# Performance work log

Measured on AMD Instinct MI355X. Metric: run time of the kernel, lower is better.

## Reference

```python
import jax, jax.numpy as jnp
import numpy as np
import math

D_MODEL = 2048
N_HEADS = 16
D_HEAD = D_MODEL // N_HEADS
D_FF = 8192
B = 2
S = 2048
LN_EPS = 1e-5


def _rope_tables(s, d_head):
    inv_freq = 1.0 / (10000.0 ** (np.arange(0, d_head, 2, dtype=np.float32) / d_head))
    t = np.arange(s, dtype=np.float32)
    freqs = np.outer(t, inv_freq)                      # [s, d_head/2]
    emb = np.concatenate([freqs, freqs], axis=-1)      # [s, d_head]
    cos = jnp.asarray(np.cos(emb))[None, None]         # [1,1,s,d_head]
    sin = jnp.asarray(np.sin(emb))[None, None]
    return cos, sin


def setup_inputs() -> dict:
    key = jax.random.key(0)
    ks = jax.random.split(key, 12)
    x = jax.random.normal(ks[0], (B, S, D_MODEL), dtype=jnp.float32)
    cos, sin = _rope_tables(S, D_HEAD)
    # additive causal mask
    mask = jnp.where(jnp.tril(jnp.ones((S, S), dtype=bool)), 0.0, -1e9).astype(jnp.float32)[None, None]
    s_in = 1.0 / math.sqrt(D_MODEL)
    s_ff = 1.0 / math.sqrt(D_FF)
    params = {
        "ln1_g": jnp.ones((D_MODEL,), jnp.float32),
        "ln1_b": jnp.zeros((D_MODEL,), jnp.float32),
        "w_qkv": jax.random.uniform(ks[1], (D_MODEL, 3 * D_MODEL), jnp.float32, -s_in, s_in),
        "b_qkv": jax.random.uniform(ks[2], (3 * D_MODEL,), jnp.float32, -s_in, s_in),
        "w_out": jax.random.uniform(ks[3], (D_MODEL, D_MODEL), jnp.float32, -s_in, s_in),
        "b_out": jax.random.uniform(ks[4], (D_MODEL,), jnp.float32, -s_in, s_in),
        "ln2_g": jnp.ones((D_MODEL,), jnp.float32),
        "ln2_b": jnp.zeros((D_MODEL,), jnp.float32),
        "w_ff1": jax.random.uniform(ks[5], (D_MODEL, D_FF), jnp.float32, -s_in, s_in),
        "b_ff1": jax.random.uniform(ks[6], (D_FF,), jnp.float32, -s_in, s_in),
        "w_ff2": jax.random.uniform(ks[7], (D_FF, D_MODEL), jnp.float32, -s_ff, s_ff),
        "b_ff2": jax.random.uniform(ks[8], (D_MODEL,), jnp.float32, -s_ff, s_ff),
    }
    return {"x": x, "cos": cos, "sin": sin, "mask": mask, **params}


def _layernorm(x, g, b):
    m = jnp.mean(x, axis=-1, keepdims=True)
    v = jnp.var(x, axis=-1, keepdims=True)
    return (x - m) * jax.lax.rsqrt(v + LN_EPS) * g + b


def _rotate_half(x):
    x1, x2 = jnp.split(x, 2, axis=-1)
    return jnp.concatenate([-x2, x1], axis=-1)


def reference(x, cos, sin, mask,
              ln1_g, ln1_b, w_qkv, b_qkv, w_out, b_out,
              ln2_g, ln2_b, w_ff1, b_ff1, w_ff2, b_ff2):
    b, s, d = x.shape
    # attention sub-block (dropout = identity, eval mode)
    xn = _layernorm(x, ln1_g, ln1_b)
    qkv = (xn @ w_qkv + b_qkv).reshape(b, s, 3, N_HEADS, D_HEAD)
    qkv = jnp.transpose(qkv, (2, 0, 3, 1, 4))           # [3,b,h,s,dh]
    q, k, v = qkv[0], qkv[1], qkv[2]
    q = q * cos + _rotate_half(q) * sin
    k = k * cos + _rotate_half(k) * sin
    scale = 1.0 / math.sqrt(D_HEAD)
    attn = jnp.einsum('bhqd,bhkd->bhqk', q, k) * scale + mask
    attn = jax.nn.softmax(attn, axis=-1)
    a_out = jnp.einsum('bhqk,bhkd->bhqd', attn, v)
    a_out = jnp.transpose(a_out, (0, 2, 1, 3)).reshape(b, s, d)
    x = x + (a_out @ w_out + b_out)
    # MLP sub-block (exact GELU, matching torch nn.GELU default)
    xn = _layernorm(x, ln2_g, ln2_b)
    h = jax.nn.gelu(xn @ w_ff1 + b_ff1, approximate=False)
    x = x + (h @ w_ff2 + b_ff2)
    return x
```

## Files before the change

### kernel.cpp

```cpp
#include <hip/hip_runtime.h>
#include <hip/hip_bf16.h>
#include <math.h>

typedef __hip_bfloat16 bf16;
using bf16x8 = __bf16 __attribute__((ext_vector_type(8)));
using f32x4  = float  __attribute__((ext_vector_type(4)));

#define D_MODEL 2048
#define S_LEN   2048
#define NB      2
#define NH      16
#define DHEAD   128
#define DFF     8192
#define M_ROWS  (NB * S_LEN)

__device__ __forceinline__ void gload_lds16(const void* g, void* l) {
    __builtin_amdgcn_global_load_lds((const __attribute__((address_space(1))) void*)g,
                                     (__attribute__((address_space(3))) void*)l, 16, 0, 0);
}

__global__ __launch_bounds__(256) void ln_kernel(const float* __restrict__ x,
                                                 const float* __restrict__ gw,
                                                 const float* __restrict__ bw,
                                                 bf16* __restrict__ out) {
    const int row = blockIdx.x;
    const float* xr = x + (size_t)row * D_MODEL;
    const int tid = threadIdx.x;
    float4 v0 = ((const float4*)xr)[tid * 2];
    float4 v1 = ((const float4*)xr)[tid * 2 + 1];
    float s = v0.x + v0.y + v0.z + v0.w + v1.x + v1.y + v1.z + v1.w;
    float q = v0.x*v0.x + v0.y*v0.y + v0.z*v0.z + v0.w*v0.w
            + v1.x*v1.x + v1.y*v1.y + v1.z*v1.z + v1.w*v1.w;
    #pragma unroll
    for (int off = 32; off; off >>= 1) {
        s += __shfl_xor(s, off);
        q += __shfl_xor(q, off);
    }
    __shared__ float red[8];
    const int wid = tid >> 6;
    if ((tid & 63) == 0) { red[wid] = s; red[4 + wid] = q; }
    __syncthreads();
    s = red[0] + red[1] + red[2] + red[3];
    q = red[4] + red[5] + red[6] + red[7];
    const float mean = s * (1.0f / D_MODEL);
    const float var  = q * (1.0f / D_MODEL) - mean * mean;
    const float inv  = rsqrtf(var + 1e-5f);
    float4 g0 = ((const float4*)gw)[tid * 2];
    float4 g1 = ((const float4*)gw)[tid * 2 + 1];
    float4 b0 = ((const float4*)bw)[tid * 2];
    float4 b1 = ((const float4*)bw)[tid * 2 + 1];
    bf16* orow = out + (size_t)row * D_MODEL + tid * 8;
    orow[0] = __float2bfloat16((v0.x - mean) * inv * g0.x + b0.x);
    orow[1] = __float2bfloat16((v0.y - mean) * inv * g0.y + b0.y);
    orow[2] = __float2bfloat16((v0.z - mean) * inv * g0.z + b0.z);
    orow[3] = __float2bfloat16((v0.w - mean) * inv * g0.w + b0.w);
    orow[4] = __float2bfloat16((v1.x - mean) * inv * g1.x + b1.x);
    orow[5] = __float2bfloat16((v1.y - mean) * inv * g1.y + b1.y);
    orow[6] = __float2bfloat16((v1.z - mean) * inv * g1.z + b1.z);
    orow[7] = __float2bfloat16((v1.w - mean) * inv * g1.w + b1.w);
}

__global__ __launch_bounds__(256) void transpose_f2b(const float* __restrict__ in,
                                                     bf16* __restrict__ out,
                                                     int R, int C) {
    __shared__ float t[32][33];
    const int c0 = blockIdx.x * 32, r0 = blockIdx.y * 32;
    const int tx = threadIdx.x & 31, ty = threadIdx.x >> 5;
    #pragma unroll
    for (int i = ty; i < 32; i += 8) t[i][tx] = in[(size_t)(r0 + i) * C + c0 + tx];
    __syncthreads();
    #pragma unroll
    for (int i = ty; i < 32; i += 8)
        out[(size_t)(c0 + i) * R + r0 + tx] = __float2bfloat16(t[tx][i]);
}

__global__ __launch_bounds__(256) void transpose_v(const bf16* __restrict__ in,
                                                   bf16* __restrict__ out) {
    const int bh = blockIdx.z;
    const bf16* ib = in + (size_t)bh * S_LEN * DHEAD;
    bf16* ob = out + (size_t)bh * DHEAD * S_LEN;
    __shared__ float t[32][33];
    const int c0 = blockIdx.x * 32;
    const int r0 = blockIdx.y * 32;
    const int tx = threadIdx.x & 31, ty = threadIdx.x >> 5;
    #pragma unroll
    for (int i = ty; i < 32; i += 8)
        t[i][tx] = __bfloat162float(ib[(size_t)(r0 + i) * DHEAD + c0 + tx]);
    __syncthreads();
    #pragma unroll
    for (int i = ty; i < 32; i += 8)
        ob[(size_t)(c0 + i) * S_LEN + r0 + tx] = __float2bfloat16(t[tx][i]);
}

__global__ __launch_bounds__(256) void rope_kernel(bf16* __restrict__ qk,
                                                   const float* __restrict__ ct,
                                                   const float* __restrict__ st) {
    const size_t idx = (size_t)blockIdx.x * 256 + threadIdx.x;
    const int dh = (int)(idx & 63);
    const size_t rrow = idx >> 6;
    const int sidx = (int)(rrow & (S_LEN - 1));
    const int which = (int)(rrow >> 16);
    const float f = (which == 0) ? 0.08838834764831845f : 1.0f;
    bf16* p = qk + rrow * DHEAD;
    const float c  = ct[sidx * DHEAD + dh];
    const float sn = st[sidx * DHEAD + dh];
    const float x1 = __bfloat162float(p[dh]);
    const float x2 = __bfloat162float(p[dh + 64]);
    p[dh]      = __float2bfloat16((x1 * c - x2 * sn) * f);
    p[dh + 64] = __float2bfloat16((x2 * c + x1 * sn) * f);
}

template <int EPI>
__global__ __launch_bounds__(256) void gemm_kernel(const bf16* __restrict__ A,
                                                   const bf16* __restrict__ Bt,
                                                   const float* __restrict__ bias,
                                                   const float* __restrict__ resid,
                                                   void* __restrict__ outp,
                                                   int M, int N, int K, int kLen) {
    __shared__ __align__(16) bf16 As[128][64];
    __shared__ __align__(16) bf16 Bs[128][64];
    const int tid  = threadIdx.x;
    const int lane = tid & 63;
    const int wid  = tid >> 6;
    const int wr = wid >> 1, wc = wid & 1;
    const int cc = lane & 15, g = lane >> 4;
    const int csw = cc & 7;

    const int nx = gridDim.x, ny = gridDim.y, nz = gridDim.z;
    int flat = blockIdx.x + nx * (blockIdx.y + ny * blockIdx.z);
    const int nwg = nx * ny * nz;
    flat = (flat & 7) * (nwg >> 3) + (flat >> 3);
    const int bx = flat % nx;
    const int t2 = flat / nx;
    const int by = t2 % ny;
    const int bz = t2 / ny;
    const int m0 = by * 128, n0 = bx * 128;
    const int kStart = bz * kLen;

    const int srow  = lane >> 3;
    const int sslot = (lane & 7) ^ (srow & 7);
    const int sb    = sslot * 16;

    f32x4 acc[4][4];
    const f32x4 zero = {0.f, 0.f, 0.f, 0.f};
    #pragma unroll
    for (int i = 0; i < 4; i++)
        #pragma unroll
        for (int j = 0; j < 4; j++) acc[i][j] = zero;

    const char* gA = (const char*)A  + ((size_t)(m0 + wid * 32 + srow) * K) * 2 + sb;
    const char* gB = (const char*)Bt + ((size_t)(n0 + wid * 32 + srow) * K) * 2 + sb;
    char* lA = (char*)&As[0][0] + wid * 4096;
    char* lB = (char*)&Bs[0][0] + wid * 4096;
    const size_t rowK2 = (size_t)K * 2;

    for (int k0 = kStart; k0 < kStart + kLen; k0 += 64) {
        #pragma unroll
        for (int c = 0; c < 4; ++c) {
            gload_lds16(gA + (size_t)k0 * 2 + (size_t)c * 8 * rowK2, lA + c * 1024);
            gload_lds16(gB + (size_t)k0 * 2 + (size_t)c * 8 * rowK2, lB + c * 1024);
        }
        __syncthreads();
        #pragma unroll
        for (int kh = 0; kh < 2; kh++) {
            const int ux = ((kh * 4 + g) ^ csw) << 4;
            bf16x8 af[4], bfm[4];
            #pragma unroll
            for (int mi = 0; mi < 4; mi++)
                af[mi]  = *(const bf16x8*)((const char*)&As[wr * 64 + mi * 16 + cc][0] + ux);
            #pragma unroll
            for (int ni = 0; ni < 4; ni++)
                bfm[ni] = *(const bf16x8*)((const char*)&Bs[wc * 64 + ni * 16 + cc][0] + ux);
            #pragma unroll
            for (int mi = 0; mi < 4; mi++)
                #pragma unroll
                for (int ni = 0; ni < 4; ni++)
                    acc[mi][ni] = __builtin_amdgcn_mfma_f32_16x16x32_bf16(af[mi], bfm[ni], acc[mi][ni], 0, 0, 0);
        }
        __syncthreads();
    }

    #pragma unroll
    for (int mi = 0; mi < 4; mi++) {
        #pragma unroll
        for (int ni = 0; ni < 4; ni++) {
            const int colb = n0 + wc * 64 + ni * 16 + cc;
            const float bcol = (EPI == 3) ? 0.0f : bias[colb];
            #pragma unroll
            for (int r = 0; r < 4; r++) {
                const int row = m0 + wr * 64 + mi * 16 + g * 4 + r;
                const float v = acc[mi][ni][r] + bcol;
                if (EPI == 0) {
                    const int which = colb >> 11;
                    const int h     = (colb >> 7) & 15;
                    const int dh    = colb & 127;
                    const int b     = row >> 11;
                    const int sidx  = row & (S_LEN - 1);
                    bf16* o = (bf16*)outp;
                    o[((size_t)(which * 32 + b * 16 + h) * S_LEN + sidx) * DHEAD + dh] = __float2bfloat16(v);
                } else if (EPI == 1) {
                    float* o = (float*)outp;
                    o[(size_t)row * N + colb] = v + resid[(size_t)row * N + colb];
                } else if (EPI == 2) {
                    bf16* o = (bf16*)outp;
                    const float gel = 0.5f * v * (1.0f + erff(v * 0.70710678118f));
                    o[(size_t)row * N + colb] = __float2bfloat16(gel);
                } else {
                    float* o = (float*)outp + (size_t)bz * M * N;
                    o[(size_t)row * N + colb] = v;
                }
            }
        }
    }
}

__global__ __launch_bounds__(256) void ff2_combine(const float* __restrict__ p,
                                                   const float* __restrict__ bias,
                                                   float* __restrict__ out) {
    const size_t i4 = (size_t)blockIdx.x * 256 + threadIdx.x;
    const float4 a  = ((const float4*)out)[i4];
    const float4 p0 = ((const float4*)p)[i4];
    const float4 p1 = ((const float4*)(p + (size_t)M_ROWS * D_MODEL))[i4];
    const float4 b  = ((const float4*)bias)[i4 & (D_MODEL / 4 - 1)];
    float4 r;
    r.x = a.x + p0.x + p1.x + b.x;
    r.y = a.y + p0.y + p1.y + b.y;
    r.z = a.z + p0.z + p1.z + b.z;
    r.w = a.w + p0.w + p1.w + b.w;
    ((float4*)out)[i4] = r;
}

__global__ __launch_bounds__(256) void attn_kernel(const bf16* __restrict__ q,
                                                   const bf16* __restrict__ k,
                                                   const bf16* __restrict__ vT,
                                                   bf16* __restrict__ aout) {
    int flat = blockIdx.x + gridDim.x * blockIdx.y;
    const int nwg = gridDim.x * gridDim.y;
    flat = (flat & 7) * (nwg >> 3) + (flat >> 3);
    const int qt = (int)(gridDim.x - 1 - (flat % gridDim.x));
    const int bh = flat / gridDim.x;
    const int tid = threadIdx.x;
    const int lane = tid & 63, wid = tid >> 6;
    const int cc = lane & 15, g = lane >> 4;
    const int csw = cc & 7;
    const int q0 = qt * 64;
    const int q0w = q0 + wid * 16;
    const bf16* qb = q  + (size_t)bh * S_LEN * DHEAD;
    const char* kb2 = (const char*)(k  + (size_t)bh * S_LEN * DHEAD);
    const char* vb2 = (const char*)(vT + (size_t)bh * DHEAD * S_LEN);

    __shared__ __align__(16) bf16 Ks[2][64][128];
    __shared__ __align__(16) bf16 Vs[2][128][64];
    __shared__ __align__(16) bf16 Ps[4][16][72];

    const int kst_row = wid * 4 + (lane >> 4);
    const int kst_sl  = (lane & 15) ^ (kst_row & 7);
    const int vst_row = wid * 8 + (lane >> 3);
    const int vst_sl  = (lane & 7) ^ (vst_row & 7);

    bf16x8 qf[4];
    #pragma unroll
    for (int kk = 0; kk < 4; kk++)
        qf[kk] = *(const bf16x8*)(qb + (size_t)(q0w + cc) * DHEAD + kk * 32 + g * 8);

    f32x4 oacc[8];
    const f32x4 zero = {0.f, 0.f, 0.f, 0.f};
    #pragma unroll
    for (int d = 0; d < 8; d++) oacc[d] = zero;
    float lsum[4] = {0.f, 0.f, 0.f, 0.f};

    {
        char* ksl = (char*)&Ks[0][0][0] + wid * 1024;
        char* vsl = (char*)&Vs[0][0][0] + wid * 1024;
        #pragma unroll
        for (int i = 0; i < 4; ++i) {
            gload_lds16(kb2 + (size_t)(kst_row + i * 16) * 256 + kst_sl * 16, ksl + i * 4096);
            gload_lds16(vb2 + (size_t)(vst_row + i * 32) * (S_LEN * 2) + vst_sl * 16, vsl + i * 4096);
        }
    }
    asm volatile("s_waitcnt vmcnt(0)" ::: "memory");
    __syncthreads();

    int cur = 0;
    for (int kt = 0; kt <= qt; ++kt) {
        const int kv0 = kt * 64;
        if (kt < qt) {
            const int nv0 = kv0 + 64;
            char* ksl = (char*)&Ks[cur ^ 1][0][0] + wid * 1024;
            char* vsl = (char*)&Vs[cur ^ 1][0][0] + wid * 1024;
            #pragma unroll
            for (int i = 0; i < 4; ++i) {
                gload_lds16(kb2 + (size_t)(nv0 + kst_row + i * 16) * 256 + kst_sl * 16, ksl + i * 4096);
                gload_lds16(vb2 + (size_t)(vst_row + i * 32) * (S_LEN * 2) + (size_t)nv0 * 2 + vst_sl * 16, vsl + i * 4096);
            }
        }

        f32x4 sacc[4];
        #pragma unroll
        for (int ni = 0; ni < 4; ni++) sacc[ni] = zero;
        __builtin_amdgcn_s_setprio(1);
        #pragma unroll
        for (int kk = 0; kk < 4; kk++) {
            const int ux = ((kk * 4 + g) ^ csw) << 4;
            #pragma unroll
            for (int ni = 0; ni < 4; ni++) {
                const bf16x8 kf = *(const bf16x8*)((const char*)&Ks[cur][ni * 16 + cc][0] + ux);
                sacc[ni] = __builtin_amdgcn_mfma_f32_16x16x32_bf16(qf[kk], kf, sacc[ni], 0, 0, 0);
            }
        }
        __builtin_amdgcn_s_setprio(0);

        #pragma unroll
        for (int r = 0; r < 4; r++) {
            const int qrow = q0w + g * 4 + r;
            float p[4];
            #pragma unroll
            for (int ni = 0; ni < 4; ni++) {
                const float sv = (kv0 + ni * 16 + cc <= qrow) ? sacc[ni][r] : -1e30f;
                p[ni] = __expf(sv);
            }
            lsum[r] += (p[0] + p[1]) + (p[2] + p[3]);
            #pragma unroll
            for (int ni = 0; ni < 4; ni++)
                Ps[wid][g * 4 + r][ni * 16 + cc] = __float2bfloat16(p[ni]);
        }

        __builtin_amdgcn_s_setprio(1);
        #pragma unroll
        for (int ks = 0; ks < 2; ks++) {
            const bf16x8 pf = *(const bf16x8*)(&Ps[wid][cc][ks * 32 + g * 8]);
            const int ux = ((ks * 4 + g) ^ csw) << 4;
            #pragma unroll
            for (int d = 0; d < 8; d++) {
                const bf16x8 vf = *(const bf16x8*)((const char*)&Vs[cur][d * 16 + cc][0] + ux);
                oacc[d] = __builtin_amdgcn_mfma_f32_16x16x32_bf16(pf, vf, oacc[d], 0, 0, 0);
            }
        }
        __builtin_amdgcn_s_setprio(0);

        asm volatile("s_waitcnt vmcnt(0)" ::: "memory");
        __syncthreads();
        cur ^= 1;
    }

    const int b = bh >> 4, h = bh & 15;
    #pragma unroll
    for (int r = 0; r < 4; r++) {
        float rs = lsum[r];
        #pragma unroll
        for (int off = 1; off < 16; off <<= 1) rs += __shfl_xor(rs, off);
        const float invl = 1.0f / rs;
        const int srow = q0w + g * 4 + r;
        bf16* orow = aout + ((size_t)(b * S_LEN + srow)) * D_MODEL + h * DHEAD;
        #pragma unroll
        for (int d = 0; d < 8; d++) orow[d * 16 + cc] = __float2bfloat16(oacc[d][r] * invl);
    }
}

extern "C" void kernel_launch(void* const* d_in, const int* in_sizes, int n_in,
                              void* d_out, int out_size, void* d_ws, size_t ws_size,
                              hipStream_t stream) {
    (void)in_sizes; (void)n_in; (void)out_size; (void)ws_size;
    const float* x      = (const float*)d_in[0];
    const float* cosb   = (const float*)d_in[1];
    const float* sinb   = (const float*)d_in[2];
    const float* ln1_g  = (const float*)d_in[4];
    const float* ln1_b  = (const float*)d_in[5];
    const float* w_qkv  = (const float*)d_in[6];
    const float* b_qkv  = (const float*)d_in[7];
    const float* w_out  = (const float*)d_in[8];
    const float* b_out  = (const float*)d_in[9];
    const float* ln2_g  = (const float*)d_in[10];
    const float* ln2_b  = (const float*)d_in[11];
    const float* w_ff1  = (const float*)d_in[12];
    const float* b_ff1  = (const float*)d_in[13];
    const float* w_ff2  = (const float*)d_in[14];
    const float* b_ff2  = (const float*)d_in[15];
    float* out = (float*)d_out;

    char* ws = (char*)d_ws;
    bf16* wT_qkv = (bf16*)(ws + 0);
    bf16* wT_out = (bf16*)(ws + 25165824);
    bf16* wT_ff1 = (bf16*)(ws + 33554432);
    bf16* wT_ff2 = (bf16*)(ws + 67108864);
    bf16* xn     = (bf16*)(ws + 100663296);
    bf16* qkv    = (bf16*)(ws + 117440512);
    bf16* aoutb  = (bf16*)(ws + 167772160);
    bf16* vTb    = (bf16*)(ws + 184549376);
    bf16* hbuf   = (bf16*)(ws + 117440512);
    float* partial = (float*)(ws + 0);
    bf16* kbuf = qkv + (size_t)32 * S_LEN * DHEAD;
    bf16* vbuf = qkv + (size_t)64 * S_LEN * DHEAD;

    transpose_f2b<<<dim3(192, 64),  256, 0, stream>>>(w_qkv, wT_qkv, 2048, 6144);
    transpose_f2b<<<dim3(64, 64),   256, 0, stream>>>(w_out, wT_out, 2048, 2048);
    transpose_f2b<<<dim3(256, 64),  256, 0, stream>>>(w_ff1, wT_ff1, 2048, 8192);
    transpose_f2b<<<dim3(64, 256),  256, 0, stream>>>(w_ff2, wT_ff2, 8192, 2048);

    ln_kernel<<<M_ROWS, 256, 0, stream>>>(x, ln1_g, ln1_b, xn);
    gemm_kernel<0><<<dim3(48, 32), 256, 0, stream>>>(xn, wT_qkv, b_qkv, nullptr, qkv, M_ROWS, 6144, 2048, 2048);
    rope_kernel<<<32768, 256, 0, stream>>>(qkv, cosb, sinb);
    transpose_v<<<dim3(4, 64, 32), 256, 0, stream>>>(vbuf, vTb);
    attn_kernel<<<dim3(32, 32), 256, 0, stream>>>(qkv, kbuf, vTb, aoutb);
    gemm_kernel<1><<<dim3(16, 32), 256, 0, stream>>>(aoutb, wT_out, b_out, x, out, M_ROWS, 2048, 2048, 2048);
    ln_kernel<<<M_ROWS, 256, 0, stream>>>(out, ln2_g, ln2_b, xn);
    gemm_kernel<2><<<dim3(64, 32), 256, 0, stream>>>(xn, wT_ff1, b_ff1, nullptr, hbuf, M_ROWS, DFF, 2048, 2048);
    gemm_kernel<3><<<dim3(16, 32, 2), 256, 0, stream>>>(hbuf, wT_ff2, nullptr, nullptr, partial, M_ROWS, 2048, 8192, 4096);
    ff2_combine<<<8192, 256, 0, stream>>>(partial, b_ff2, out);
}
```

Before: 799.4 us.

## Add 256x256-tile GEMM kernel with 8 waves and phased LDS pipelining

Adds a new gemm256 kernel that uses 256x256 output tiles with 512 threads, double-buffered LDS filled by direct global-to-LDS loads, XOR swizzling, and a workgroup index remap for cache locality. Each K-step is split into four phases that overlap MFMA compute with staging the next tile, using explicit vmcnt waits and barriers. The QKV, FF1 and FF2 GEMMs switch to it, while the old kernel is specialized to the residual epilogue for the output projection. The larger tiles cut global traffic per flop, but they also mean fewer blocks and more register pressure. The hand-tuned wait counts could introduce ordering bugs.

Result: faster. 712.7 us (-10.8%).

```diff
diff --git a/kernel.cpp b/kernel.cpp
--- a/kernel.cpp
+++ b/kernel.cpp
@@ -185,11 +185,141 @@
         #pragma unroll
         for (int ni = 0; ni < 4; ni++) {
             const int colb = n0 + wc * 64 + ni * 16 + cc;
-            const float bcol = (EPI == 3) ? 0.0f : bias[colb];
+            const float bcol = bias[colb];
             #pragma unroll
             for (int r = 0; r < 4; r++) {
                 const int row = m0 + wr * 64 + mi * 16 + g * 4 + r;
                 const float v = acc[mi][ni][r] + bcol;
+                float* o = (float*)outp;
+                o[(size_t)row * N + colb] = v + resid[(size_t)row * N + colb];
+            }
+        }
+    }
+}
+
+template <int EPI>
+__global__ __launch_bounds__(512, 2) void gemm256(const bf16* __restrict__ A,
+                                                  const bf16* __restrict__ Bt,
+                                                  const float* __restrict__ bias,
+                                                  void* __restrict__ outp,
+                                                  int M, int N, int K, int kLen) {
+    __shared__ __align__(16) bf16 lds[2][2][2][128][64];
+    const int tid  = threadIdx.x;
+    const int lane = tid & 63;
+    const int wid  = tid >> 6;
+    const int wave_m = wid >> 2, wave_n = wid & 3;
+    const int wm16 = wave_m * 16, wn16 = wave_n * 16;
+    const int cc = lane & 15, g = lane >> 4;
+    const int csw = cc & 7;
+
+    const int nx = gridDim.x, ny = gridDim.y, nz = gridDim.z;
+    int flat = blockIdx.x + nx * (blockIdx.y + ny * blockIdx.z);
+    const int nwg = nx * ny * nz;
+    flat = (flat & 7) * (nwg >> 3) + (flat >> 3);
+    const int bx = flat % nx;
+    const int t2 = flat / nx;
+    const int by = t2 % ny;
+    const int bz = t2 / ny;
+    const int m0 = by * 256, n0 = bx * 256;
+    const int kStart = bz * kLen;
+    const int NT = kLen >> 6;
+
+    const int srow_lo = tid >> 3;
+    const int sbyte   = ((tid & 7) ^ (srow_lo & 7)) * 16;
+    const size_t rowB  = (size_t)K * 2;
+    const size_t halfB = rowB * 128;
+    const size_t jB    = rowB * 64;
+    const char* sA = (const char*)A  + (size_t)(m0 + srow_lo) * rowB + sbyte;
+    const char* sB = (const char*)Bt + (size_t)(n0 + srow_lo) * rowB + sbyte;
+
+#define STAGE(SOP, SMH, P, K0) do {                                           \
+    const char* _s = (SOP ? sB : sA) + (size_t)(SMH) * halfB + (size_t)(K0) * 2; \
+    char* _d = ((char*)&lds[P][SOP][SMH][0][0]) + wid * 1024;                 \
+    gload_lds16(_s, _d);                                                      \
+    gload_lds16(_s + jB, _d + 8192);                                          \
+} while (0)
+
+    f32x4 acc[8][4];
+    const f32x4 zero = {0.f, 0.f, 0.f, 0.f};
+    #pragma unroll
+    for (int i = 0; i < 8; i++)
+        #pragma unroll
+        for (int j = 0; j < 4; j++) acc[i][j] = zero;
+
+#define LDA(PB, MH, MI, UX) (*(const bf16x8*)((const char*)&lds[PB][0][MH][(MI) * 32 + wm16 + cc][0] + (UX)))
+#define LDB(PB, NH, NI, UX) (*(const bf16x8*)((const char*)&lds[PB][1][NH][(NI) * 64 + wn16 + cc][0] + (UX)))
+#define MFMA(a, b, c) __builtin_amdgcn_mfma_f32_16x16x32_bf16(a, b, c, 0, 0, 0)
+
+#define PHASE(PB, MH, NH, DOST, SOP, SMH, VN) do {                            \
+    __builtin_amdgcn_s_setprio(1);                                            \
+    _Pragma("unroll")                                                         \
+    for (int kk = 0; kk < 2; ++kk) {                                          \
+        const int ux = ((kk * 4 + g) ^ csw) << 4;                             \
+        const bf16x8 b0 = LDB(PB, NH, 0, ux);                                 \
+        const bf16x8 b1 = LDB(PB, NH, 1, ux);                                 \
+        const bf16x8 a0 = LDA(PB, MH, 0, ux);                                 \
+        const bf16x8 a1 = LDA(PB, MH, 1, ux);                                 \
+        const bf16x8 a2 = LDA(PB, MH, 2, ux);                                 \
+        const bf16x8 a3 = LDA(PB, MH, 3, ux);                                 \
+        acc[(MH)*4+0][(NH)*2+0] = MFMA(a0, b0, acc[(MH)*4+0][(NH)*2+0]);      \
+        acc[(MH)*4+1][(NH)*2+0] = MFMA(a1, b0, acc[(MH)*4+1][(NH)*2+0]);      \
+        acc[(MH)*4+2][(NH)*2+0] = MFMA(a2, b0, acc[(MH)*4+2][(NH)*2+0]);      \
+        acc[(MH)*4+3][(NH)*2+0] = MFMA(a3, b0, acc[(MH)*4+3][(NH)*2+0]);      \
+        acc[(MH)*4+0][(NH)*2+1] = MFMA(a0, b1, acc[(MH)*4+0][(NH)*2+1]);      \
+        acc[(MH)*4+1][(NH)*2+1] = MFMA(a1, b1, acc[(MH)*4+1][(NH)*2+1]);      \
+        acc[(MH)*4+2][(NH)*2+1] = MFMA(a2, b1, acc[(MH)*4+2][(NH)*2+1]);      \
+        acc[(MH)*4+3][(NH)*2+1] = MFMA(a3, b1, acc[(MH)*4+3][(NH)*2+1]);      \
+    }                                                                         \
+    __builtin_amdgcn_s_setprio(0);                                            \
+    if (DOST) STAGE(SOP, SMH, (PB) ^ 1, k0n);                                 \
+    __builtin_amdgcn_sched_barrier(0);                                        \
+    asm volatile("s_waitcnt vmcnt(" VN ")" ::: "memory");                     \
+    __builtin_amdgcn_s_barrier();                                             \
+    __builtin_amdgcn_sched_barrier(0);                                        \
+} while (0)
+
+    STAGE(0, 0, 0, kStart);
+    STAGE(1, 0, 0, kStart);
+    STAGE(0, 1, 0, kStart);
+    STAGE(1, 1, 0, kStart);
+    __builtin_amdgcn_sched_barrier(0);
+    asm volatile("s_waitcnt vmcnt(4)" ::: "memory");
+    __builtin_amdgcn_s_barrier();
+    __builtin_amdgcn_sched_barrier(0);
+
+    for (int t = 0; t < NT - 1; ++t) {
+        const int PB = t & 1;
+        const int k0n = kStart + (t + 1) * 64;
+        PHASE(PB, 0, 0, true, 0, 0, "4");
+        PHASE(PB, 1, 0, true, 1, 0, "4");
+        PHASE(PB, 0, 1, true, 0, 1, "6");
+        PHASE(PB, 1, 1, true, 1, 1, "4");
+    }
+    {
+        const int PB = (NT - 1) & 1;
+        const int k0n = 0; (void)k0n;
+        PHASE(PB, 0, 0, false, 0, 0, "2");
+        PHASE(PB, 1, 0, false, 1, 0, "0");
+        PHASE(PB, 0, 1, false, 0, 1, "0");
+        PHASE(PB, 1, 1, false, 1, 1, "0");
+    }
+#undef PHASE
+#undef LDA
+#undef LDB
+#undef MFMA
+#undef STAGE
+
+    #pragma unroll
+    for (int ai = 0; ai < 8; ai++) {
+        const int rowb = m0 + (ai >> 2) * 128 + (ai & 3) * 32 + wm16 + g * 4;
+        #pragma unroll
+        for (int bj = 0; bj < 4; bj++) {
+            const int colb = n0 + (bj >> 1) * 128 + (bj & 1) * 64 + wn16 + cc;
+            const float bcol = (EPI == 3) ? 0.0f : bias[colb];
+            #pragma unroll
+            for (int r = 0; r < 4; r++) {
+                const int row = rowb + r;
+                const float v = acc[ai][bj][r] + bcol;
                 if (EPI == 0) {
                     const int which = colb >> 11;
                     const int h     = (colb >> 7) & 15;
@@ -198,9 +328,6 @@
                     const int sidx  = row & (S_LEN - 1);
                     bf16* o = (bf16*)outp;
                     o[((size_t)(which * 32 + b * 16 + h) * S_LEN + sidx) * DHEAD + dh] = __float2bfloat16(v);
-                } else if (EPI == 1) {
-                    float* o = (float*)outp;
-                    o[(size_t)row * N + colb] = v + resid[(size_t)row * N + colb];
                 } else if (EPI == 2) {
                     bf16* o = (bf16*)outp;
                     const float gel = 0.5f * v * (1.0f + erff(v * 0.70710678118f));
@@ -398,13 +525,13 @@
     transpose_f2b<<<dim3(64, 256),  256, 0, stream>>>(w_ff2, wT_ff2, 8192, 2048);
 
     ln_kernel<<<M_ROWS, 256, 0, stream>>>(x, ln1_g, ln1_b, xn);
-    gemm_kernel<0><<<dim3(48, 32), 256, 0, stream>>>(xn, wT_qkv, b_qkv, nullptr, qkv, M_ROWS, 6144, 2048, 2048);
+    gemm256<0><<<dim3(24, 16), 512, 0, stream>>>(xn, wT_qkv, b_qkv, qkv, M_ROWS, 6144, 2048, 2048);
     rope_kernel<<<32768, 256, 0, stream>>>(qkv, cosb, sinb);
     transpose_v<<<dim3(4, 64, 32), 256, 0, stream>>>(vbuf, vTb);
     attn_kernel<<<dim3(32, 32), 256, 0, stream>>>(qkv, kbuf, vTb, aoutb);
     gemm_kernel<1><<<dim3(16, 32), 256, 0, stream>>>(aoutb, wT_out, b_out, x, out, M_ROWS, 2048, 2048, 2048);
     ln_kernel<<<M_ROWS, 256, 0, stream>>>(out, ln2_g, ln2_b, xn);
-    gemm_kernel<2><<<dim3(64, 32), 256, 0, stream>>>(xn, wT_ff1, b_ff1, nullptr, hbuf, M_ROWS, DFF, 2048, 2048);
-    gemm_kernel<3><<<dim3(16, 32, 2), 256, 0, stream>>>(hbuf, wT_ff2, nullptr, nullptr, partial, M_ROWS, 2048, 8192, 4096);
+    gemm256<2><<<dim3(32, 16), 512, 0, stream>>>(xn, wT_ff1, b_ff1, hbuf, M_ROWS, DFF, 2048, 2048);
+    gemm256<3><<<dim3(8, 16, 2), 512, 0, stream>>>(hbuf, wT_ff2, nullptr, partial, M_ROWS, 2048, 8192, 4096);
     ff2_combine<<<8192, 256, 0, stream>>>(partial, b_ff2, out);
 }
```
